# Performance work log

Hardware: AMD Instinct MI355X
Metric: run time of the kernel (lower is better)

## Reference

```python
import jax, jax.numpy as jnp
import numpy as np

N_HEAD = 16
N_EMBD = 1024
B, T = 4, 2048


def setup_inputs() -> dict:
    key = jax.random.key(0)
    k1, k2, k3, k4, k5 = jax.random.split(key, 5)
    x = jax.random.normal(k1, (B, T, N_EMBD), dtype=jnp.float32)
    # Linear params (torch nn.Linear: y = x @ W.T + b); store as [in, out] for einsum
    s = 1.0 / np.sqrt(N_EMBD)
    W_qkv = jax.random.uniform(k2, (N_EMBD, 3 * N_EMBD), minval=-s, maxval=s, dtype=jnp.float32)
    b_qkv = jax.random.uniform(k3, (3 * N_EMBD,), minval=-s, maxval=s, dtype=jnp.float32)
    W_out = jax.random.uniform(k4, (N_EMBD, N_EMBD), minval=-s, maxval=s, dtype=jnp.float32)
    b_out = jax.random.uniform(k5, (N_EMBD,), minval=-s, maxval=s, dtype=jnp.float32)
    return {"x": x, "W_qkv": W_qkv, "b_qkv": b_qkv, "W_out": W_out, "b_out": b_out}


def reference(x, W_qkv, b_qkv, W_out, b_out):
    Bv, Tv, C = x.shape
    H = N_HEAD
    d_k = C // H
    qkv = x @ W_qkv + b_qkv                      # [B,T,3C]
    q, k, v = jnp.split(qkv, 3, axis=-1)
    # [B,T,C] -> [B,H,T,d_k]
    def to_heads(t):
        return t.reshape(Bv, Tv, H, d_k).transpose(0, 2, 1, 3)
    q, k, v = to_heads(q), to_heads(k), to_heads(v)
    scores = jnp.einsum('bhqd,bhkd->bhqk', q, k) / jnp.sqrt(jnp.float32(d_k))
    causal = jnp.tril(jnp.ones((Tv, Tv), dtype=bool))  # True = keep
    scores = jnp.where(causal, scores, jnp.float32(-jnp.inf))
    attn = jax.nn.softmax(scores, axis=-1)
    out = jnp.einsum('bhqk,bhkd->bhqd', attn, v)       # [B,H,T,d_k]
    out = out.transpose(0, 2, 1, 3).reshape(Bv, Tv, C)
    return out @ W_out + b_out
```

## Files before the change

### kernel.cpp

```cpp
#include <hip/hip_runtime.h>

#define T_SEQ 2048
#define NBATCH 4
#define NHEAD 16
#define DKH 64
#define CEMB 1024

typedef unsigned short u16;
typedef __attribute__((ext_vector_type(8))) short short8;
typedef __attribute__((ext_vector_type(8))) unsigned short ushort8v;
typedef __attribute__((ext_vector_type(4))) float f32x4;

__device__ __forceinline__ u16 f2bf(float f) {
  unsigned int x = __builtin_bit_cast(unsigned int, f);
  x += 0x7FFFu + ((x >> 16) & 1u);
  return (u16)(x >> 16);
}

__device__ __forceinline__ void async_copy16(const void* g, void* lds) {
  __builtin_amdgcn_global_load_lds(
      (const __attribute__((address_space(1))) void*)g,
      (__attribute__((address_space(3))) void*)lds, 16, 0, 0);
}

__global__ __launch_bounds__(256) void k_convert(const float* __restrict__ in,
                                                 u16* __restrict__ out, int n8) {
  int i = blockIdx.x * 256 + threadIdx.x;
  if (i >= n8) return;
  const float4* p = (const float4*)in;
  float4 a = p[2 * i], b = p[2 * i + 1];
  ushort8v v;
  v[0] = f2bf(a.x); v[1] = f2bf(a.y); v[2] = f2bf(a.z); v[3] = f2bf(a.w);
  v[4] = f2bf(b.x); v[5] = f2bf(b.y); v[6] = f2bf(b.z); v[7] = f2bf(b.w);
  ((ushort8v*)out)[i] = v;
}

__global__ __launch_bounds__(256) void k_transpose(const float* __restrict__ W,
                                                   u16* __restrict__ WT, int R, int C) {
  __shared__ float tile[32][33];
  int c0 = blockIdx.x * 32, r0 = blockIdx.y * 32;
  int tx = threadIdx.x & 31;
  int ty = threadIdx.x >> 5;
#pragma unroll
  for (int i = 0; i < 4; ++i) {
    int r = ty + i * 8;
    tile[r][tx] = W[(size_t)(r0 + r) * C + c0 + tx];
  }
  __syncthreads();
#pragma unroll
  for (int i = 0; i < 4; ++i) {
    int cc = ty + i * 8;
    WT[(size_t)(c0 + cc) * R + r0 + tx] = f2bf(tile[tx][cc]);
  }
}

template <int EPI>
__global__ __launch_bounds__(256) void k_gemm_bt(
    const u16* __restrict__ A, const u16* __restrict__ BT, const float* __restrict__ bias,
    float* __restrict__ Cf, u16* __restrict__ Qb, u16* __restrict__ Kb, u16* __restrict__ Vtb,
    int M, int N, int K) {
  __shared__ u16 As[128 * 32];
  __shared__ u16 Bs[128 * 32];
  const int tid = threadIdx.x;
  const int w = tid >> 6, l = tid & 63;
  const int g = l >> 4, lr = l & 15;
  const int m0 = blockIdx.y * 128, n0 = blockIdx.x * 128;
  const int wr = (w >> 1) * 64, wc = (w & 1) * 64;
  f32x4 acc[4][4] = {};

  const int srow = l >> 2;
  const int scol = (l & 3) << 3;
  const u16* Ag = A + (size_t)m0 * K + scol;
  const u16* Bg = BT + (size_t)n0 * K + scol;

  for (int k0 = 0; k0 < K; k0 += 32) {
#pragma unroll
    for (int i = 0; i < 2; ++i) {
      int blk = i * 4 + w;
      int row = blk * 16 + srow;
      async_copy16(Ag + (size_t)row * K + k0, &As[blk * 512]);
      async_copy16(Bg + (size_t)row * K + k0, &Bs[blk * 512]);
    }
    __syncthreads();
    short8 af[4], bf[4];
#pragma unroll
    for (int mi = 0; mi < 4; ++mi)
      af[mi] = *(const short8*)&As[(wr + mi * 16 + lr) * 32 + g * 8];
#pragma unroll
    for (int ni = 0; ni < 4; ++ni)
      bf[ni] = *(const short8*)&Bs[(wc + ni * 16 + lr) * 32 + g * 8];
#pragma unroll
    for (int mi = 0; mi < 4; ++mi)
#pragma unroll
      for (int ni = 0; ni < 4; ++ni)
        acc[mi][ni] = __builtin_amdgcn_mfma_f32_16x16x32_bf16(af[mi], bf[ni], acc[mi][ni], 0, 0, 0);
    __syncthreads();
  }

  if constexpr (EPI == 0) {
#pragma unroll
    for (int mi = 0; mi < 4; ++mi) {
#pragma unroll
      for (int ni = 0; ni < 4; ++ni) {
        int ng = n0 + wc + ni * 16 + lr;
        float bs = bias[ng];
#pragma unroll
        for (int r = 0; r < 4; ++r) {
          int mg = m0 + wr + mi * 16 + g * 4 + r;
          Cf[(size_t)mg * N + ng] = acc[mi][ni][r] + bs;
        }
      }
    }
  } else {
#pragma unroll
    for (int mi = 0; mi < 4; ++mi) {
      int mg0 = m0 + wr + mi * 16 + g * 4;
      int b = mg0 >> 11;
      int t = mg0 & (T_SEQ - 1);
#pragma unroll
      for (int ni = 0; ni < 4; ++ni) {
        int ng = n0 + wc + ni * 16 + lr;
        float bs = bias[ng];
        int sect = ng >> 10;
        int nm = ng & 1023;
        int h = nm >> 6, d = nm & 63;
        u16 bv[4];
#pragma unroll
        for (int r = 0; r < 4; ++r) bv[r] = f2bf(acc[mi][ni][r] + bs);
        size_t hb = (size_t)b * NHEAD + h;
        if (sect == 0) {
          u16* q = Qb + (hb * T_SEQ + t) * DKH + d;
#pragma unroll
          for (int r = 0; r < 4; ++r) q[(size_t)r * DKH] = bv[r];
        } else if (sect == 1) {
          u16* kk = Kb + (hb * T_SEQ + t) * DKH + d;
#pragma unroll
          for (int r = 0; r < 4; ++r) kk[(size_t)r * DKH] = bv[r];
        } else {
          u16* vp = Vtb + (hb * DKH + d) * T_SEQ + t;
          ushort4 v4;
          v4.x = bv[0]; v4.y = bv[1]; v4.z = bv[2]; v4.w = bv[3];
          *(ushort4*)vp = v4;
        }
      }
    }
  }
}

__global__ __launch_bounds__(256, 2) void k_attn(const u16* __restrict__ Qb,
                                                 const u16* __restrict__ Kb,
                                                 const u16* __restrict__ Vtb,
                                                 u16* __restrict__ Ob) {
  __shared__ u16 Ks[2][64 * 64];
  __shared__ u16 Vs[2][64 * 64];
  __shared__ u16 Ps[4][32 * 72];
  const int tid = threadIdx.x;
  const int w = tid >> 6, l = tid & 63;
  const int g = l >> 4, lr = l & 15;
  const int bh = blockIdx.y;
  const int b = bh >> 4, h = bh & 15;
  const int j = blockIdx.x;
  const int qtB = 15 - j;
  const int q0a = j * 128 + w * 32;
  const int q0b = qtB * 128 + w * 32;
  const u16* Qg = Qb + (size_t)bh * T_SEQ * DKH;
  const u16* Kg = Kb + (size_t)bh * T_SEQ * DKH;
  const u16* Vg = Vtb + (size_t)bh * DKH * T_SEQ;

  const u16* KgL[2];
  const u16* VgL[2];
  int blkArr[2];
#pragma unroll
  for (int i = 0; i < 2; ++i) {
    int blk = i * 4 + w;
    blkArr[i] = blk;
    int x = blk * 1024 + l * 16;
    int c = x ^ (((x >> 7) & 7) << 4);
    int crow = c >> 7;
    int ccolb = c & 127;
    KgL[i] = Kg + crow * DKH + (ccolb >> 1);
    VgL[i] = Vg + (size_t)crow * T_SEQ + (ccolb >> 1);
  }

  auto STAGE = [&](int bufi, int kv0) {
#pragma unroll
    for (int i = 0; i < 2; ++i) {
      async_copy16(KgL[i] + (size_t)kv0 * DKH, &Ks[bufi][blkArr[i] * 512]);
      async_copy16(VgL[i] + kv0, &Vs[bufi][blkArr[i] * 512]);
    }
  };

  STAGE(0, 0);

  short8 qfrA[2][2], qfrB[2][2];
#pragma unroll
  for (int qi = 0; qi < 2; ++qi)
#pragma unroll
    for (int ka = 0; ka < 2; ++ka) {
      qfrA[qi][ka] = *(const short8*)&Qg[(size_t)(q0a + qi * 16 + lr) * DKH + ka * 32 + g * 8];
      qfrB[qi][ka] = *(const short8*)&Qg[(size_t)(q0b + qi * 16 + lr) * DKH + ka * 32 + g * 8];
    }

  f32x4 oA[2][4] = {}, oB[2][4] = {};
  float mA[2][4], lpA[2][4], mB[2][4], lpB[2][4];
#pragma unroll
  for (int qi = 0; qi < 2; ++qi)
#pragma unroll
    for (int r = 0; r < 4; ++r) {
      mA[qi][r] = -1e30f; lpA[qi][r] = 0.f;
      mB[qi][r] = -1e30f; lpB[qi][r] = 0.f;
    }

  __syncthreads();

  short8 kf[4][2], vf[4][2];
  auto tile_compute = [&](int q0w_, auto& qfr_, auto& o_, auto& m__, auto& lp_, int kv0) {
    const bool diag = (kv0 + 63 > q0w_);
    f32x4 s[2][4] = {};
    __builtin_amdgcn_s_setprio(1);
#pragma unroll
    for (int qi = 0; qi < 2; ++qi)
#pragma unroll
      for (int kv = 0; kv < 4; ++kv)
#pragma unroll
        for (int ka = 0; ka < 2; ++ka)
          s[qi][kv] = __builtin_amdgcn_mfma_f32_16x16x32_bf16(qfr_[qi][ka], kf[kv][ka], s[qi][kv], 0, 0, 0);
    __builtin_amdgcn_s_setprio(0);

    if (diag) {
#pragma unroll
      for (int qi = 0; qi < 2; ++qi)
#pragma unroll
        for (int kv = 0; kv < 4; ++kv)
#pragma unroll
          for (int r = 0; r < 4; ++r) {
            int qq = q0w_ + qi * 16 + g * 4 + r;
            int kk = kv0 + kv * 16 + lr;
            if (kk > qq) s[qi][kv][r] = -1e30f;
          }
    }

    float pmx[2][4];
    bool grow = false;
#pragma unroll
    for (int qi = 0; qi < 2; ++qi)
#pragma unroll
      for (int r = 0; r < 4; ++r) {
        float v = fmaxf(fmaxf(s[qi][0][r], s[qi][1][r]), fmaxf(s[qi][2][r], s[qi][3][r]));
        pmx[qi][r] = v;
        grow = grow || (v > m__[qi][r] + 64.f);
      }
    if (__any(grow)) {
#pragma unroll
      for (int qi = 0; qi < 2; ++qi)
#pragma unroll
        for (int r = 0; r < 4; ++r) {
          float v = pmx[qi][r];
          v = fmaxf(v, __shfl_xor(v, 1));
          v = fmaxf(v, __shfl_xor(v, 2));
          v = fmaxf(v, __shfl_xor(v, 4));
          v = fmaxf(v, __shfl_xor(v, 8));
          float mn = fmaxf(m__[qi][r], v);
          float al = __expf((m__[qi][r] - mn) * 0.125f);
          m__[qi][r] = mn;
          lp_[qi][r] *= al;
#pragma unroll
          for (int df = 0; df < 4; ++df) o_[qi][df][r] *= al;
        }
    }

#pragma unroll
    for (int qi = 0; qi < 2; ++qi)
#pragma unroll
      for (int r = 0; r < 4; ++r) {
        float mm = m__[qi][r];
        float p0 = __expf((s[qi][0][r] - mm) * 0.125f);
        float p1 = __expf((s[qi][1][r] - mm) * 0.125f);
        float p2 = __expf((s[qi][2][r] - mm) * 0.125f);
        float p3 = __expf((s[qi][3][r] - mm) * 0.125f);
        lp_[qi][r] += (p0 + p1) + (p2 + p3);
        u16* base = &Ps[w][(qi * 16 + g * 4 + r) * 72 + lr];
        base[0]  = f2bf(p0);
        base[16] = f2bf(p1);
        base[32] = f2bf(p2);
        base[48] = f2bf(p3);
      }

    short8 pf[2][2];
#pragma unroll
    for (int qi = 0; qi < 2; ++qi)
#pragma unroll
      for (int ka = 0; ka < 2; ++ka)
        pf[qi][ka] = *(const short8*)&Ps[w][(qi * 16 + lr) * 72 + ka * 32 + g * 8];
    __builtin_amdgcn_s_setprio(1);
#pragma unroll
    for (int qi = 0; qi < 2; ++qi)
#pragma unroll
      for (int df = 0; df < 4; ++df)
#pragma unroll
        for (int ka = 0; ka < 2; ++ka)
          o_[qi][df] = __builtin_amdgcn_mfma_f32_16x16x32_bf16(pf[qi][ka], vf[df][ka], o_[qi][df], 0, 0, 0);
    __builtin_amdgcn_s_setprio(0);
  };

  const int ntile = 2 * qtB + 2;
  for (int kt = 0; kt < ntile; ++kt) {
    const int cur = kt & 1;
    const int kv0 = kt * 64;
    if (kt + 1 < ntile) STAGE(cur ^ 1, kv0 + 64);

    const bool actA = (kv0 <= q0a);
    const bool actB = (kv0 <= q0b);
    if (actB) {
      const char* KsB = (const char*)Ks[cur];
      const char* VsB = (const char*)Vs[cur];
#pragma unroll
      for (int kv = 0; kv < 4; ++kv)
#pragma unroll
        for (int ka = 0; ka < 2; ++ka) {
          int row = kv * 16 + lr;
          int cidx = row * 128 + ka * 64 + g * 16;
          int x = cidx ^ ((row & 7) << 4);
          kf[kv][ka] = *(const short8*)(KsB + x);
          vf[kv][ka] = *(const short8*)(VsB + x);
        }
      if (actA) tile_compute(q0a, qfrA, oA, mA, lpA, kv0);
      tile_compute(q0b, qfrB, oB, mB, lpB, kv0);
    }

    __syncthreads();
  }

#pragma unroll
  for (int qi = 0; qi < 2; ++qi)
#pragma unroll
    for (int r = 0; r < 4; ++r) {
      float va = lpA[qi][r];
      va += __shfl_xor(va, 1); va += __shfl_xor(va, 2);
      va += __shfl_xor(va, 4); va += __shfl_xor(va, 8);
      float inva = 1.0f / va;
      int tqa = q0a + qi * 16 + g * 4 + r;
      size_t basea = ((size_t)b * T_SEQ + tqa) * CEMB + h * 64;
#pragma unroll
      for (int df = 0; df < 4; ++df)
        Ob[basea + df * 16 + lr] = f2bf(oA[qi][df][r] * inva);

      float vb = lpB[qi][r];
      vb += __shfl_xor(vb, 1); vb += __shfl_xor(vb, 2);
      vb += __shfl_xor(vb, 4); vb += __shfl_xor(vb, 8);
      float invb = 1.0f / vb;
      int tqb = q0b + qi * 16 + g * 4 + r;
      size_t baseb = ((size_t)b * T_SEQ + tqb) * CEMB + h * 64;
#pragma unroll
      for (int df = 0; df < 4; ++df)
        Ob[baseb + df * 16 + lr] = f2bf(oB[qi][df][r] * invb);
    }
}

extern "C" void kernel_launch(void* const* d_in, const int* in_sizes, int n_in,
                              void* d_out, int out_size, void* d_ws, size_t ws_size,
                              hipStream_t stream) {
  const float* x = (const float*)d_in[0];
  const float* Wqkv = (const float*)d_in[1];
  const float* bqkv = (const float*)d_in[2];
  const float* Wout = (const float*)d_in[3];
  const float* bout = (const float*)d_in[4];
  float* out = (float*)d_out;

  char* ws = (char*)d_ws;
  u16* xb  = (u16*)(ws + 0);
  u16* WqT = (u16*)(ws + 16777216);
  u16* WoT = (u16*)(ws + 23068672);
  u16* Qb  = (u16*)(ws + 25165824);
  u16* Kb  = (u16*)(ws + 41943040);
  u16* Vtb = (u16*)(ws + 58720256);
  u16* Ob  = (u16*)(ws + 75497472);

  k_convert<<<4096, 256, 0, stream>>>(x, xb, (NBATCH * T_SEQ * CEMB) / 8);
  k_transpose<<<dim3(96, 32), 256, 0, stream>>>(Wqkv, WqT, 1024, 3072);
  k_transpose<<<dim3(32, 32), 256, 0, stream>>>(Wout, WoT, 1024, 1024);
  k_gemm_bt<1><<<dim3(24, 64), 256, 0, stream>>>(xb, WqT, bqkv, nullptr, Qb, Kb, Vtb,
                                                 NBATCH * T_SEQ, 3 * CEMB, CEMB);
  k_attn<<<dim3(8, 64), 256, 0, stream>>>(Qb, Kb, Vtb, Ob);
  k_gemm_bt<0><<<dim3(8, 64), 256, 0, stream>>>(Ob, WoT, bout, out, nullptr, nullptr, nullptr,
                                                NBATCH * T_SEQ, CEMB, CEMB);
}
```

Measured before the change: 294.1 us.

## Halve attention query tile per wave, double grid, raise occupancy, swizzle P buffer

The attention kernel now gives each wave 16 query rows instead of 32, uses 64-row query blocks paired across the causal diagonal (32 tiles), and launches twice as many blocks with launch bounds raised to 4 blocks per CU. The P scratch buffer moves from a padded layout to an XOR-swizzled 64-wide layout, which saves LDS. The aim is more parallelism and occupancy to hide latency and fix tail imbalance. The cost is less K/V reuse per staged tile, so LDS loads and global K/V traffic per query roughly double.

```diff
diff --git a/kernel.cpp b/kernel.cpp
--- a/kernel.cpp
+++ b/kernel.cpp
@@ -147,25 +147,26 @@
   }
 }
 
-__global__ __launch_bounds__(256, 2) void k_attn(const u16* __restrict__ Qb,
+__global__ __launch_bounds__(256, 4) void k_attn(const u16* __restrict__ Qb,
                                                  const u16* __restrict__ Kb,
                                                  const u16* __restrict__ Vtb,
                                                  u16* __restrict__ Ob) {
   __shared__ u16 Ks[2][64 * 64];
   __shared__ u16 Vs[2][64 * 64];
-  __shared__ u16 Ps[4][32 * 72];
+  __shared__ u16 Ps[4 * 16 * 64];
   const int tid = threadIdx.x;
   const int w = tid >> 6, l = tid & 63;
   const int g = l >> 4, lr = l & 15;
   const int bh = blockIdx.y;
   const int b = bh >> 4, h = bh & 15;
-  const int j = blockIdx.x;
-  const int qtB = 15 - j;
-  const int q0a = j * 128 + w * 32;
-  const int q0b = qtB * 128 + w * 32;
+  const int jA = blockIdx.x;
+  const int jB = 31 - jA;
+  const int q0a = jA * 64 + w * 16;
+  const int q0b = jB * 64 + w * 16;
   const u16* Qg = Qb + (size_t)bh * T_SEQ * DKH;
   const u16* Kg = Kb + (size_t)bh * T_SEQ * DKH;
   const u16* Vg = Vtb + (size_t)bh * DKH * T_SEQ;
+  u16* PsW = &Ps[w * 1024];
 
   const u16* KgL[2];
   const u16* VgL[2];
@@ -192,169 +193,149 @@
 
   STAGE(0, 0);
 
-  short8 qfrA[2][2], qfrB[2][2];
-#pragma unroll
-  for (int qi = 0; qi < 2; ++qi)
-#pragma unroll
-    for (int ka = 0; ka < 2; ++ka) {
-      qfrA[qi][ka] = *(const short8*)&Qg[(size_t)(q0a + qi * 16 + lr) * DKH + ka * 32 + g * 8];
-      qfrB[qi][ka] = *(const short8*)&Qg[(size_t)(q0b + qi * 16 + lr) * DKH + ka * 32 + g * 8];
-    }
-
-  f32x4 oA[2][4] = {}, oB[2][4] = {};
-  float mA[2][4], lpA[2][4], mB[2][4], lpB[2][4];
-#pragma unroll
-  for (int qi = 0; qi < 2; ++qi)
+  short8 qfrA[2], qfrB[2];
+#pragma unroll
+  for (int ka = 0; ka < 2; ++ka) {
+    qfrA[ka] = *(const short8*)&Qg[(size_t)(q0a + lr) * DKH + ka * 32 + g * 8];
+    qfrB[ka] = *(const short8*)&Qg[(size_t)(q0b + lr) * DKH + ka * 32 + g * 8];
+  }
+
+  f32x4 oA[4] = {}, oB[4] = {};
+  float mA[4], lpA[4], mB[4], lpB[4];
+#pragma unroll
+  for (int r = 0; r < 4; ++r) {
+    mA[r] = -1e30f; lpA[r] = 0.f;
+    mB[r] = -1e30f; lpB[r] = 0.f;
+  }
+
+  __syncthreads();
+
+  short8 kf[4][2], vf[4][2];
+  auto tile_compute = [&](int q0w_, short8 (&qfr_)[2], f32x4 (&o_)[4],
+                          float (&m__)[4], float (&lp_)[4], int kv0) {
+    const bool diag = (kv0 + 63 > q0w_);
+    f32x4 s[4] = {};
+    __builtin_amdgcn_s_setprio(1);
+#pragma unroll
+    for (int kv = 0; kv < 4; ++kv)
+#pragma unroll
+      for (int ka = 0; ka < 2; ++ka)
+        s[kv] = __builtin_amdgcn_mfma_f32_16x16x32_bf16(qfr_[ka], kf[kv][ka], s[kv], 0, 0, 0);
+    __builtin_amdgcn_s_setprio(0);
+
+    if (diag) {
+#pragma unroll
+      for (int kv = 0; kv < 4; ++kv)
+#pragma unroll
+        for (int r = 0; r < 4; ++r) {
+          int qq = q0w_ + g * 4 + r;
+          int kk = kv0 + kv * 16 + lr;
+          if (kk > qq) s[kv][r] = -1e30f;
+        }
+    }
+
+    float pmx[4];
+    bool grow = false;
 #pragma unroll
     for (int r = 0; r < 4; ++r) {
-      mA[qi][r] = -1e30f; lpA[qi][r] = 0.f;
-      mB[qi][r] = -1e30f; lpB[qi][r] = 0.f;
-    }
-
-  __syncthreads();
-
-  short8 kf[4][2], vf[4][2];
-  auto tile_compute = [&](int q0w_, auto& qfr_, auto& o_, auto& m__, auto& lp_, int kv0) {
-    const bool diag = (kv0 + 63 > q0w_);
-    f32x4 s[2][4] = {};
+      float v = fmaxf(fmaxf(s[0][r], s[1][r]), fmaxf(s[2][r], s[3][r]));
+      pmx[r] = v;
+      grow = grow || (v > m__[r] + 64.f);
+    }
+    if (__any(grow)) {
+#pragma unroll
+      for (int r = 0; r < 4; ++r) {
+        float v = pmx[r];
+        v = fmaxf(v, __shfl_xor(v, 1));
+        v = fmaxf(v, __shfl_xor(v, 2));
+        v = fmaxf(v, __shfl_xor(v, 4));
+        v = fmaxf(v, __shfl_xor(v, 8));
+        float mn = fmaxf(m__[r], v);
+        float al = __expf((m__[r] - mn) * 0.125f);
+        m__[r] = mn;
+        lp_[r] *= al;
+#pragma unroll
+        for (int df = 0; df < 4; ++df) o_[df][r] *= al;
+      }
+    }
+
+#pragma unroll
+    for (int r = 0; r < 4; ++r) {
+      float mm = m__[r];
+      float p0 = __expf((s[0][r] - mm) * 0.125f);
+      float p1 = __expf((s[1][r] - mm) * 0.125f);
+      float p2 = __expf((s[2][r] - mm) * 0.125f);
+      float p3 = __expf((s[3][r] - mm) * 0.125f);
+      lp_[r] += (p0 + p1) + (p2 + p3);
+      int row4 = g * 4 + r;
+      char* rowp = (char*)PsW + row4 * 128;
+      int mk = (row4 & 7) << 4;
+      *(u16*)(rowp + ((0 * 32 + lr * 2) ^ mk)) = f2bf(p0);
+      *(u16*)(rowp + ((1 * 32 + lr * 2) ^ mk)) = f2bf(p1);
+      *(u16*)(rowp + ((2 * 32 + lr * 2) ^ mk)) = f2bf(p2);
+      *(u16*)(rowp + ((3 * 32 + lr * 2) ^ mk)) = f2bf(p3);
+    }
+
+    short8 pf[2];
+    const int mkr = (lr & 7) << 4;
+#pragma unroll
+    for (int ka = 0; ka < 2; ++ka)
+      pf[ka] = *(const short8*)((char*)PsW + ((lr * 128 + ka * 64 + g * 16) ^ mkr));
     __builtin_amdgcn_s_setprio(1);
 #pragma unroll
-    for (int qi = 0; qi < 2; ++qi)
-#pragma unroll
-      for (int kv = 0; kv < 4; ++kv)
-#pragma unroll
-        for (int ka = 0; ka < 2; ++ka)
-          s[qi][kv] = __builtin_amdgcn_mfma_f32_16x16x32_bf16(qfr_[qi][ka], kf[kv][ka], s[qi][kv], 0, 0, 0);
-    __builtin_amdgcn_s_setprio(0);
-
-    if (diag) {
-#pragma unroll
-      for (int qi = 0; qi < 2; ++qi)
-#pragma unroll
-        for (int kv = 0; kv < 4; ++kv)
-#pragma unroll
-          for (int r = 0; r < 4; ++r) {
-            int qq = q0w_ + qi * 16 + g * 4 + r;
-            int kk = kv0 + kv * 16 + lr;
-            if (kk > qq) s[qi][kv][r] = -1e30f;
-          }
-    }
-
-    float pmx[2][4];
-    bool grow = false;
-#pragma unroll
-    for (int qi = 0; qi < 2; ++qi)
-#pragma unroll
-      for (int r = 0; r < 4; ++r) {
-        float v = fmaxf(fmaxf(s[qi][0][r], s[qi][1][r]), fmaxf(s[qi][2][r], s[qi][3][r]));
-        pmx[qi][r] = v;
-        grow = grow || (v > m__[qi][r] + 64.f);
-      }
-    if (__any(grow)) {
-#pragma unroll
-      for (int qi = 0; qi < 2; ++qi)
-#pragma unroll
-        for (int r = 0; r < 4; ++r) {
-          float v = pmx[qi][r];
-          v = fmaxf(v, __shfl_xor(v, 1));
-          v = fmaxf(v, __shfl_xor(v, 2));
-          v = fmaxf(v, __shfl_xor(v, 4));
-          v = fmaxf(v, __shfl_xor(v, 8));
-          float mn = fmaxf(m__[qi][r], v);
-          float al = __expf((m__[qi][r] - mn) * 0.125f);
-          m__[qi][r] = mn;
-          lp_[qi][r] *= al;
-#pragma unroll
-          for (int df = 0; df < 4; ++df) o_[qi][df][r] *= al;
-        }
-    }
-
-#pragma unroll
-    for (int qi = 0; qi < 2; ++qi)
-#pragma unroll
-      for (int r = 0; r < 4; ++r) {
-        float mm = m__[qi][r];
-        float p0 = __expf((s[qi][0][r] - mm) * 0.125f);
-        float p1 = __expf((s[qi][1][r] - mm) * 0.125f);
-        float p2 = __expf((s[qi][2][r] - mm) * 0.125f);
-        float p3 = __expf((s[qi][3][r] - mm) * 0.125f);
-        lp_[qi][r] += (p0 + p1) + (p2 + p3);
-        u16* base = &Ps[w][(qi * 16 + g * 4 + r) * 72 + lr];
-        base[0]  = f2bf(p0);
-        base[16] = f2bf(p1);
-        base[32] = f2bf(p2);
-        base[48] = f2bf(p3);
-      }
-
-    short8 pf[2][2];
-#pragma unroll
-    for (int qi = 0; qi < 2; ++qi)
+    for (int df = 0; df < 4; ++df)
 #pragma unroll
       for (int ka = 0; ka < 2; ++ka)
-        pf[qi][ka] = *(const short8*)&Ps[w][(qi * 16 + lr) * 72 + ka * 32 + g * 8];
-    __builtin_amdgcn_s_setprio(1);
-#pragma unroll
-    for (int qi = 0; qi < 2; ++qi)
-#pragma unroll
-      for (int df = 0; df < 4; ++df)
-#pragma unroll
-        for (int ka = 0; ka < 2; ++ka)
-          o_[qi][df] = __builtin_amdgcn_mfma_f32_16x16x32_bf16(pf[qi][ka], vf[df][ka], o_[qi][df], 0, 0, 0);
+        o_[df] = __builtin_amdgcn_mfma_f32_16x16x32_bf16(pf[ka], vf[df][ka], o_[df], 0, 0, 0);
     __builtin_amdgcn_s_setprio(0);
   };
 
-  const int ntile = 2 * qtB + 2;
+  const int ntile = jB + 1;
   for (int kt = 0; kt < ntile; ++kt) {
     const int cur = kt & 1;
     const int kv0 = kt * 64;
     if (kt + 1 < ntile) STAGE(cur ^ 1, kv0 + 64);
 
-    const bool actA = (kv0 <= q0a);
-    const bool actB = (kv0 <= q0b);
-    if (actB) {
-      const char* KsB = (const char*)Ks[cur];
-      const char* VsB = (const char*)Vs[cur];
-#pragma unroll
-      for (int kv = 0; kv < 4; ++kv)
-#pragma unroll
-        for (int ka = 0; ka < 2; ++ka) {
-          int row = kv * 16 + lr;
-          int cidx = row * 128 + ka * 64 + g * 16;
-          int x = cidx ^ ((row & 7) << 4);
-          kf[kv][ka] = *(const short8*)(KsB + x);
-          vf[kv][ka] = *(const short8*)(VsB + x);
-        }
-      if (actA) tile_compute(q0a, qfrA, oA, mA, lpA, kv0);
-      tile_compute(q0b, qfrB, oB, mB, lpB, kv0);
-    }
+    const char* KsB = (const char*)Ks[cur];
+    const char* VsB = (const char*)Vs[cur];
+#pragma unroll
+    for (int kv = 0; kv < 4; ++kv)
+#pragma unroll
+      for (int ka = 0; ka < 2; ++ka) {
+        int row = kv * 16 + lr;
+        int cidx = row * 128 + ka * 64 + g * 16;
+        int x = cidx ^ ((row & 7) << 4);
+        kf[kv][ka] = *(const short8*)(KsB + x);
+        vf[kv][ka] = *(const short8*)(VsB + x);
+      }
+    if (kt <= jA) tile_compute(q0a, qfrA, oA, mA, lpA, kv0);
+    tile_compute(q0b, qfrB, oB, mB, lpB, kv0);
 
     __syncthreads();
   }
 
 #pragma unroll
-  for (int qi = 0; qi < 2; ++qi)
-#pragma unroll
-    for (int r = 0; r < 4; ++r) {
-      float va = lpA[qi][r];
-      va += __shfl_xor(va, 1); va += __shfl_xor(va, 2);
-      va += __shfl_xor(va, 4); va += __shfl_xor(va, 8);
-      float inva = 1.0f / va;
-      int tqa = q0a + qi * 16 + g * 4 + r;
-      size_t basea = ((size_t)b * T_SEQ + tqa) * CEMB + h * 64;
-#pragma unroll
-      for (int df = 0; df < 4; ++df)
-        Ob[basea + df * 16 + lr] = f2bf(oA[qi][df][r] * inva);
-
-      float vb = lpB[qi][r];
-      vb += __shfl_xor(vb, 1); vb += __shfl_xor(vb, 2);
-      vb += __shfl_xor(vb, 4); vb += __shfl_xor(vb, 8);
-      float invb = 1.0f / vb;
-      int tqb = q0b + qi * 16 + g * 4 + r;
-      size_t baseb = ((size_t)b * T_SEQ + tqb) * CEMB + h * 64;
-#pragma unroll
-      for (int df = 0; df < 4; ++df)
-        Ob[baseb + df * 16 + lr] = f2bf(oB[qi][df][r] * invb);
-    }
+  for (int r = 0; r < 4; ++r) {
+    float va = lpA[r];
+    va += __shfl_xor(va, 1); va += __shfl_xor(va, 2);
+    va += __shfl_xor(va, 4); va += __shfl_xor(va, 8);
+    float inva = 1.0f / va;
+    int tqa = q0a + g * 4 + r;
+    size_t basea = ((size_t)b * T_SEQ + tqa) * CEMB + h * 64;
+#pragma unroll
+    for (int df = 0; df < 4; ++df)
+      Ob[basea + df * 16 + lr] = f2bf(oA[df][r] * inva);
+
+    float vb = lpB[r];
+    vb += __shfl_xor(vb, 1); vb += __shfl_xor(vb, 2);
+    vb += __shfl_xor(vb, 4); vb += __shfl_xor(vb, 8);
+    float invb = 1.0f / vb;
+    int tqb = q0b + g * 4 + r;
+    size_t baseb = ((size_t)b * T_SEQ + tqb) * CEMB + h * 64;
+#pragma unroll
+    for (int df = 0; df < 4; ++df)
+      Ob[baseb + df * 16 + lr] = f2bf(oB[df][r] * invb);
+  }
 }
 
 extern "C" void kernel_launch(void* const* d_in, const int* in_sizes, int n_in,
@@ -381,7 +362,7 @@
   k_transpose<<<dim3(32, 32), 256, 0, stream>>>(Wout, WoT, 1024, 1024);
   k_gemm_bt<1><<<dim3(24, 64), 256, 0, stream>>>(xb, WqT, bqkv, nullptr, Qb, Kb, Vtb,
                                                  NBATCH * T_SEQ, 3 * CEMB, CEMB);
-  k_attn<<<dim3(8, 64), 256, 0, stream>>>(Qb, Kb, Vtb, Ob);
+  k_attn<<<dim3(16, 64), 256, 0, stream>>>(Qb, Kb, Vtb, Ob);
   k_gemm_bt<0><<<dim3(8, 64), 256, 0, stream>>>(Ob, WoT, bout, out, nullptr, nullptr, nullptr,
                                                 NBATCH * T_SEQ, CEMB, CEMB);
 }
```

Measured after the change: 745.6 us. 2.54x slower.
